# Kernel optimization log

Measured on AMD Instinct MI355X. Metric: run time of the kernel, lower is better.

The kernel has to match this reference:

```python
import jax, jax.numpy as jnp
import numpy as np

N_NODES = 40000
N_EDGES = 640000
D = 128
N_GRAPHS = 64


def gcn_conv(x, W, b, edge_index):
    """PyG-style GCNConv: add self-loops, symmetric norm, linear, scatter-add."""
    n = x.shape[0]
    loops = jnp.arange(n, dtype=edge_index.dtype)
    src = jnp.concatenate([edge_index[0], loops])  # message sources (x_j)
    dst = jnp.concatenate([edge_index[1], loops])  # aggregation targets
    # deg computed over targets (col) with unit edge weights, incl. self-loops
    deg = jax.ops.segment_sum(jnp.ones_like(src, dtype=x.dtype), dst, num_segments=n)
    dinv = jnp.where(deg > 0, jax.lax.rsqrt(jnp.maximum(deg, 1.0)), 0.0)
    norm = dinv[src] * dinv[dst]  # [E+N]
    h = x @ W  # [N, d_out]
    out = jax.ops.segment_sum(norm[:, None] * h[src], dst, num_segments=n)
    return out + b


def global_mean_pool(x, batch, num_graphs):
    summed = jax.ops.segment_sum(x, batch, num_segments=num_graphs)
    counts = jax.ops.segment_sum(jnp.ones((x.shape[0],), x.dtype), batch, num_segments=num_graphs)
    return summed / jnp.maximum(counts, 1.0)[:, None]


def setup_inputs() -> dict:
    key = jax.random.key(0)
    ks = jax.random.split(key, 6)
    x = jax.random.normal(ks[0], (N_NODES, D), dtype=jnp.float32)
    edge_index = jax.random.randint(ks[1], (2, N_EDGES), 0, N_NODES)
    batch = jnp.sort(jax.random.randint(ks[2], (N_NODES,), 0, N_GRAPHS))
    s = 1.0 / np.sqrt(D)
    W1 = jax.random.normal(ks[3], (D, D), dtype=jnp.float32) * s
    W2 = jax.random.normal(ks[4], (D, D), dtype=jnp.float32) * s
    b1 = jnp.zeros((D,), jnp.float32)
    b2 = jnp.zeros((D,), jnp.float32)
    return {"x": x, "edge_index": edge_index, "batch": batch,
            "W1": W1, "b1": b1, "W2": W2, "b2": b2}


def reference(x, edge_index, batch, W1, b1, W2, b2):
    h = jax.nn.relu(gcn_conv(x, W1, b1, edge_index))
    h = gcn_conv(h, W2, b2, edge_index)  # no ReLU on last layer
    return global_mean_pool(h, batch, N_GRAPHS)
```

## Files before the change

### kernel.cpp

```cpp
#include <hip/hip_runtime.h>

#define D 128
#define N_GRAPHS 64

typedef unsigned int uint32;
typedef __attribute__((ext_vector_type(8))) _Float16 f16x8;
typedef __attribute__((ext_vector_type(4))) float f32x4;

__device__ __forceinline__ float hl(uint32 u) {
    return (float)__builtin_bit_cast(_Float16, (unsigned short)(u & 0xFFFF));
}
__device__ __forceinline__ float hh(uint32 u) {
    return (float)__builtin_bit_cast(_Float16, (unsigned short)(u >> 16));
}
__device__ __forceinline__ uint32 h2pair(float a, float b) {
    unsigned short ua = __builtin_bit_cast(unsigned short, (_Float16)a);
    unsigned short ub = __builtin_bit_cast(unsigned short, (_Float16)b);
    return (uint32)ua | ((uint32)ub << 16);
}

__global__ __launch_bounds__(256) void prep_kernel(int* __restrict__ cnt,
                                                   const float* __restrict__ W1,
                                                   uint32* __restrict__ Wh, int n) {
    int i = blockIdx.x * 256 + threadIdx.x;
    if (i < n) {
        cnt[i] = 0;
    } else if (i < n + D * (D / 2)) {
        int j = i - n;
        int nn = j & 127, kd = j >> 7;
        float v0 = W1[(size_t)(2 * kd) * D + nn];
        float v1 = W1[(size_t)(2 * kd + 1) * D + nn];
        Wh[nn * 64 + kd] = h2pair(v0, v1);
    }
}


#define GBM 64

__global__ __launch_bounds__(256) void count_gemm_kernel(
    const float* __restrict__ A, const uint32* __restrict__ Wh,
    uint32* __restrict__ hb, int M, int gemmBlocks,
    const int* __restrict__ dst, int* __restrict__ cnt,
    int* __restrict__ rank, int E) {
    __shared__ uint32 lds[64 * 68];

    if (blockIdx.x >= gemmBlocks) {
        int e = (blockIdx.x - gemmBlocks) * 256 + threadIdx.x;
        if (e < E) rank[e] = atomicAdd(&cnt[dst[e]], 1);
        return;
    }

    uint32* As = lds;
    int tid = threadIdx.x;
    int row0 = blockIdx.x * GBM;

#pragma unroll
    for (int j = 0; j < 8; ++j) {
        int idx = tid + j * 256;
        int r = idx >> 5, c4 = idx & 31;
        float4 v = make_float4(0.f, 0.f, 0.f, 0.f);
        if (row0 + r < M) v = *(const float4*)&A[(size_t)(row0 + r) * D + c4 * 4];
        As[r * 68 + c4 * 2 + 0] = h2pair(v.x, v.y);
        As[r * 68 + c4 * 2 + 1] = h2pair(v.z, v.w);
    }
    __syncthreads();

    int wave = tid >> 6, lane = tid & 63;
    int quad = lane >> 4, l16 = lane & 15;
    int wr = (wave & 1) * 32;
    int wc = (wave >> 1) * 64;
    f32x4 acc[2][4];
#pragma unroll
    for (int mi = 0; mi < 2; ++mi)
#pragma unroll
        for (int ni = 0; ni < 4; ++ni) acc[mi][ni] = (f32x4){0.f, 0.f, 0.f, 0.f};

#pragma unroll
    for (int ks = 0; ks < 4; ++ks) {
        int kd = ks * 16 + quad * 4;
        f16x8 a0 = *(f16x8*)&As[(wr + l16) * 68 + kd];
        f16x8 a1 = *(f16x8*)&As[(wr + 16 + l16) * 68 + kd];
        f16x8 b0 = *(const f16x8*)&Wh[(wc + l16) * 64 + kd];
        f16x8 b1 = *(const f16x8*)&Wh[(wc + 16 + l16) * 64 + kd];
        f16x8 b2 = *(const f16x8*)&Wh[(wc + 32 + l16) * 64 + kd];
        f16x8 b3 = *(const f16x8*)&Wh[(wc + 48 + l16) * 64 + kd];
        acc[0][0] = __builtin_amdgcn_mfma_f32_16x16x32_f16(a0, b0, acc[0][0], 0, 0, 0);
        acc[0][1] = __builtin_amdgcn_mfma_f32_16x16x32_f16(a0, b1, acc[0][1], 0, 0, 0);
        acc[0][2] = __builtin_amdgcn_mfma_f32_16x16x32_f16(a0, b2, acc[0][2], 0, 0, 0);
        acc[0][3] = __builtin_amdgcn_mfma_f32_16x16x32_f16(a0, b3, acc[0][3], 0, 0, 0);
        acc[1][0] = __builtin_amdgcn_mfma_f32_16x16x32_f16(a1, b0, acc[1][0], 0, 0, 0);
        acc[1][1] = __builtin_amdgcn_mfma_f32_16x16x32_f16(a1, b1, acc[1][1], 0, 0, 0);
        acc[1][2] = __builtin_amdgcn_mfma_f32_16x16x32_f16(a1, b2, acc[1][2], 0, 0, 0);
        acc[1][3] = __builtin_amdgcn_mfma_f32_16x16x32_f16(a1, b3, acc[1][3], 0, 0, 0);
    }
    __syncthreads();

    unsigned short* cs = (unsigned short*)lds;
#pragma unroll
    for (int mi = 0; mi < 2; ++mi)
#pragma unroll
        for (int ni = 0; ni < 4; ++ni)
#pragma unroll
            for (int r = 0; r < 4; ++r) {
                int row = wr + mi * 16 + quad * 4 + r;
                int col2 = wc + ni * 16 + l16;
                cs[row * 128 + col2] =
                    __builtin_bit_cast(unsigned short, (_Float16)acc[mi][ni][r]);
            }
    __syncthreads();
#pragma unroll
    for (int j = 0; j < 4; ++j) {
        int idx = tid + j * 256;
        int r = idx >> 4, q = idx & 15;
        if (row0 + r < M)
            *(uint4*)&hb[(size_t)(row0 + r) * 64 + q * 4] = *(uint4*)&lds[r * 64 + q * 4];
    }
}


__global__ __launch_bounds__(1024) void scanA_kernel(const int* __restrict__ cnt,
                                                     int* __restrict__ rowptr,
                                                     int* __restrict__ tot,
                                                     float* __restrict__ dinv,
                                                     float* __restrict__ c,
                                                     const int* __restrict__ batch, int n) {
    __shared__ int swave[16];
    int t = threadIdx.x;
    int lane = t & 63, wave = t >> 6;
    int i = blockIdx.x * 1024 + t;
    {
        size_t f4base = (size_t)blockIdx.x * 1024 * 16;
        size_t f4lim = (size_t)n * 16;
        float4 z = make_float4(0.f, 0.f, 0.f, 0.f);
#pragma unroll
        for (int q = 0; q < 16; ++q) {
            size_t idx = f4base + (size_t)q * 1024 + t;
            if (idx < f4lim) ((float4*)c)[idx] = z;
        }
    }
    int orig = (i < n) ? cnt[i] : 0;
    int v = orig;
#pragma unroll
    for (int off = 1; off < 64; off <<= 1) {
        int u = __shfl_up(v, off, 64);
        if (lane >= off) v += u;
    }
    if (lane == 63) swave[wave] = v;
    __syncthreads();
    if (wave == 0) {
        int wv = (lane < 16) ? swave[lane] : 0;
#pragma unroll
        for (int off = 1; off < 16; off <<= 1) {
            int u = __shfl_up(wv, off, 64);
            if (lane >= off) wv += u;
        }
        if (lane < 16) swave[lane] = wv;
    }
    if (i < n) {
        float dv = rsqrtf((float)(orig + 1));
        dinv[i] = dv;
        c[(size_t)i * N_GRAPHS + batch[i]] = dv * dv;
    }
    __syncthreads();
    int incl = v + ((wave > 0) ? swave[wave - 1] : 0);
    if (i < n) rowptr[i] = incl - orig;
    if (t == 1023) tot[blockIdx.x] = incl;
}

__global__ __launch_bounds__(1024) void scanB_kernel(int* __restrict__ rowptr,
                                                     const int* __restrict__ tot,
                                                     int n, int nchunks) {
    __shared__ int soff;
    int b = blockIdx.x, t = threadIdx.x;
    if (t == 0) {
        int o = 0;
        for (int j = 0; j < b; ++j) o += tot[j];
        soff = o;
    }
    __syncthreads();
    int i = b * 1024 + t;
    if (i < n) rowptr[i] += soff;
    if (b == 0 && t == 0) {
        int o = 0;
        for (int j = 0; j < nchunks; ++j) o += tot[j];
        rowptr[n] = o;
    }
}

__global__ void fill_kernel(const int* __restrict__ src, const int* __restrict__ dst,
                            const int* __restrict__ rowptr, const int* __restrict__ rank,
                            int* __restrict__ col, int E) {
    int e = blockIdx.x * blockDim.x + threadIdx.x;
    if (e < E) col[rowptr[dst[e]] + rank[e]] = src[e];
}


__global__ __launch_bounds__(128) void agg_kernel(const uint32* __restrict__ hb,
                                                  const int* __restrict__ rowptr,
                                                  const int* __restrict__ col,
                                                  const float* __restrict__ dinv,
                                                  const float* __restrict__ bias,
                                                  const int* __restrict__ batch,
                                                  float* __restrict__ c,
                                                  uint32* __restrict__ h1, int n) {
    int tid = threadIdx.x;
    int lane32 = tid & 31;
    int slot = tid >> 5;
    int node = blockIdx.x * 4 + slot;
    if (node >= n) return;
    const uint2* __restrict__ h2 = (const uint2*)hb;

    float di = dinv[node];
    int bg = batch[node];
    float ws = di * di;
    uint2 su = h2[(size_t)node * 32 + lane32];
    float a0 = ws * hl(su.x), a1 = ws * hh(su.x);
    float a2 = ws * hl(su.y), a3 = ws * hh(su.y);

    int k = rowptr[node], end = rowptr[node + 1];
    for (; k + 8 <= end; k += 8) {
        uint2 v[8];
        float w[8];
#pragma unroll
        for (int j = 0; j < 8; ++j) {
            int s = col[k + j];
            w[j] = dinv[s] * di;
            v[j] = h2[(size_t)s * 32 + lane32];
            if (lane32 == j) atomicAdd(&c[(size_t)s * N_GRAPHS + bg], w[j]);
        }
#pragma unroll
        for (int j = 0; j < 8; ++j) {
            a0 = fmaf(w[j], hl(v[j].x), a0);
            a1 = fmaf(w[j], hh(v[j].x), a1);
            a2 = fmaf(w[j], hl(v[j].y), a2);
            a3 = fmaf(w[j], hh(v[j].y), a3);
        }
    }
    for (; k < end; ++k) {
        int s = col[k];
        float w = dinv[s] * di;
        uint2 v = h2[(size_t)s * 32 + lane32];
        if (lane32 == 0) atomicAdd(&c[(size_t)s * N_GRAPHS + bg], w);
        a0 = fmaf(w, hl(v.x), a0);
        a1 = fmaf(w, hh(v.x), a1);
        a2 = fmaf(w, hl(v.y), a2);
        a3 = fmaf(w, hh(v.y), a3);
    }

    float4 b4 = ((const float4*)bias)[lane32];
    a0 = fmaxf(a0 + b4.x, 0.f);
    a1 = fmaxf(a1 + b4.y, 0.f);
    a2 = fmaxf(a2 + b4.z, 0.f);
    a3 = fmaxf(a3 + b4.w, 0.f);
    uint2 o;
    o.x = h2pair(a0, a1);
    o.y = h2pair(a2, a3);
    ((uint2*)h1)[(size_t)node * 32 + lane32] = o;
}


#define GP_NB 256
#define GP_T 16

__global__ __launch_bounds__(256) void gp_kernel(const float* __restrict__ c,
                                                 const uint32* __restrict__ H1,
                                                 float* __restrict__ Ppart, int n) {
    __shared__ float sc[GP_T][N_GRAPHS];
    __shared__ uint32 sh[GP_T][64];
    int t = threadIdx.x;
    int b = blockIdx.x;
    int jpb = (n + GP_NB - 1) / GP_NB;
    int j0 = b * jpb;
    int j1 = min(j0 + jpb, n);
    int g0 = (t & 7) * 8;
    int f0 = (t >> 3) * 4;
    float acc[8][4];
#pragma unroll
    for (int a = 0; a < 8; ++a)
#pragma unroll
        for (int q = 0; q < 4; ++q) acc[a][q] = 0.f;

    for (int jt = j0; jt < j1; jt += GP_T) {
        int cnt = min(GP_T, j1 - jt);
        {
            int r = t >> 4, q = t & 15;
            float4 v = (r < cnt) ? *(const float4*)&c[(size_t)(jt + r) * N_GRAPHS + q * 4]
                                 : make_float4(0.f, 0.f, 0.f, 0.f);
            *(float4*)&sc[r][q * 4] = v;
        }
        {
            int r = t >> 4, q = t & 15;
            uint4 v = make_uint4(0, 0, 0, 0);
            if (r < cnt) v = *(const uint4*)&H1[(size_t)(jt + r) * 64 + q * 4];
            *(uint4*)&sh[r][q * 4] = v;
        }
        __syncthreads();
#pragma unroll
        for (int r = 0; r < GP_T; ++r) {
            float cw[8], hv[4];
            *(float4*)&cw[0] = *(float4*)&sc[r][g0];
            *(float4*)&cw[4] = *(float4*)&sc[r][g0 + 4];
            uint32 u0 = sh[r][f0 >> 1], u1 = sh[r][(f0 >> 1) + 1];
            hv[0] = hl(u0); hv[1] = hh(u0); hv[2] = hl(u1); hv[3] = hh(u1);
#pragma unroll
            for (int a = 0; a < 8; ++a)
#pragma unroll
                for (int q = 0; q < 4; ++q) acc[a][q] = fmaf(cw[a], hv[q], acc[a][q]);
        }
        __syncthreads();
    }
    float* P = &Ppart[(size_t)b * N_GRAPHS * D];
#pragma unroll
    for (int a = 0; a < 8; ++a)
        *(float4*)&P[(size_t)(g0 + a) * D + f0] =
            make_float4(acc[a][0], acc[a][1], acc[a][2], acc[a][3]);
}

__global__ __launch_bounds__(256) void out_kernel(const float* __restrict__ Ppart,
                                                  const float* __restrict__ W2,
                                                  const float* __restrict__ b2,
                                                  const int* __restrict__ batch, int n,
                                                  float* __restrict__ out) {
    __shared__ float gs[D];
    __shared__ float part[2][D];
    __shared__ float srinv;
    int g = blockIdx.x, t = threadIdx.x;
    int f = t & 127, half = t >> 7;
    if (t == 0) {
        int lo = 0, hi = n;
        while (lo < hi) { int mid = (lo + hi) >> 1; if (batch[mid] < g) lo = mid + 1; else hi = mid; }
        int lb = lo;
        int g1 = g + 1;
        lo = 0; hi = n;
        while (lo < hi) { int mid = (lo + hi) >> 1; if (batch[mid] < g1) lo = mid + 1; else hi = mid; }
        int cg = lo - lb;
        srinv = (cg > 0) ? 1.0f / (float)cg : 0.0f;
    }
    float s = 0.f;
    int b0 = half * (GP_NB / 2);
#pragma unroll 8
    for (int b = b0; b < b0 + GP_NB / 2; ++b)
        s += Ppart[((size_t)b * N_GRAPHS + g) * D + f];
    part[half][f] = s;
    __syncthreads();
    if (half == 0) gs[f] = part[0][f] + part[1][f];
    __syncthreads();
    float acc = 0.f;
    int k0 = half * (D / 2);
#pragma unroll 8
    for (int k = k0; k < k0 + D / 2; ++k) acc = fmaf(gs[k], W2[k * D + f], acc);
    part[half][f] = acc;
    __syncthreads();
    if (half == 0) {
        float a = part[0][f] + part[1][f];
        float r = srinv;
        out[g * D + f] = (r > 0.f) ? fmaf(a, r, b2[f]) : 0.f;
    }
}


extern "C" void kernel_launch(void* const* d_in, const int* in_sizes, int n_in,
                              void* d_out, int out_size, void* d_ws, size_t ws_size,
                              hipStream_t stream) {
    const float* x  = (const float*)d_in[0];
    const int*   ei = (const int*)d_in[1];
    const int*   batch = (const int*)d_in[2];
    const float* W1 = (const float*)d_in[3];
    const float* b1 = (const float*)d_in[4];
    const float* W2 = (const float*)d_in[5];
    const float* b2 = (const float*)d_in[6];
    float* out = (float*)d_out;

    const int n = in_sizes[2];
    const int E = in_sizes[1] / 2;
    const int* src = ei;
    const int* dst = ei + E;

    char* ws = (char*)d_ws;
    size_t off = 0;
    auto carve = [&](size_t bytes) {
        size_t o = off;
        off = (off + bytes + 255) & ~(size_t)255;
        return (void*)(ws + o);
    };
    int*    cnt    = (int*)carve((size_t)n * 4);
    int*    rowptr = (int*)carve((size_t)(n + 1) * 4);
    float*  dinv   = (float*)carve((size_t)n * 4);
    int*    col    = (int*)carve((size_t)E * 4);
    uint32* hb     = (uint32*)carve((size_t)n * D * 2);
    uint32* h1     = (uint32*)carve((size_t)n * D * 2);
    float*  c      = (float*)carve((size_t)n * N_GRAPHS * 4);
    int*    tot    = (int*)carve(64 * 4);
    int*    rank   = (int*)carve((size_t)E * 4);
    uint32* Wh     = (uint32*)carve((size_t)D * (D / 2) * 4);
    float*  Ppart  = (float*)hb;
    (void)ws_size;

    const int nchunks = (n + 1023) >> 10;

    prep_kernel<<<(n + D * (D / 2) + 255) / 256, 256, 0, stream>>>(cnt, W1, Wh, n);

    const int gemmBlocks = (n + GBM - 1) / GBM;
    const int countBlocks = (E + 255) / 256;
    count_gemm_kernel<<<gemmBlocks + countBlocks, 256, 0, stream>>>(
        x, Wh, hb, n, gemmBlocks, dst, cnt, rank, E);

    scanA_kernel<<<nchunks, 1024, 0, stream>>>(cnt, rowptr, tot, dinv, c, batch, n);
    scanB_kernel<<<nchunks, 1024, 0, stream>>>(rowptr, tot, n, nchunks);
    fill_kernel<<<(E + 255) / 256, 256, 0, stream>>>(src, dst, rowptr, rank, col, E);

    agg_kernel<<<(n + 3) / 4, 128, 0, stream>>>(hb, rowptr, col, dinv, b1, batch, c, h1, n);

    gp_kernel<<<GP_NB, 256, 0, stream>>>(c, h1, Ppart, n);
    out_kernel<<<N_GRAPHS, 256, 0, stream>>>(Ppart, W2, b2, batch, n, out);
}
```

Before: 228.9 us.

## Replace pooled-coefficient matrix with direct second-layer aggregation into per-graph pools

The old path folded the second aggregation into a dense node-by-graph coefficient matrix. That matrix was zeroed in the scan kernel, filled by scattered atomics inside the first aggregation and then contracted with h1 in gp_kernel. The new path drops that matrix and adds a kernel that, for each graph slice, re-walks the CSR neighbours of its nodes and sums the normalised messages into a shared-memory pool. The per-slice pool partials are then reduced in out_kernel. This removes the 10 MB zero/fill, the atomics and the dense contraction, but costs a second full edge gather over h1.

```diff
diff --git a/kernel.cpp b/kernel.cpp
--- a/kernel.cpp
+++ b/kernel.cpp
@@ -121,23 +121,11 @@
 __global__ __launch_bounds__(1024) void scanA_kernel(const int* __restrict__ cnt,
                                                      int* __restrict__ rowptr,
                                                      int* __restrict__ tot,
-                                                     float* __restrict__ dinv,
-                                                     float* __restrict__ c,
-                                                     const int* __restrict__ batch, int n) {
+                                                     float* __restrict__ dinv, int n) {
     __shared__ int swave[16];
     int t = threadIdx.x;
     int lane = t & 63, wave = t >> 6;
     int i = blockIdx.x * 1024 + t;
-    {
-        size_t f4base = (size_t)blockIdx.x * 1024 * 16;
-        size_t f4lim = (size_t)n * 16;
-        float4 z = make_float4(0.f, 0.f, 0.f, 0.f);
-#pragma unroll
-        for (int q = 0; q < 16; ++q) {
-            size_t idx = f4base + (size_t)q * 1024 + t;
-            if (idx < f4lim) ((float4*)c)[idx] = z;
-        }
-    }
     int orig = (i < n) ? cnt[i] : 0;
     int v = orig;
 #pragma unroll
@@ -156,11 +144,7 @@
         }
         if (lane < 16) swave[lane] = wv;
     }
-    if (i < n) {
-        float dv = rsqrtf((float)(orig + 1));
-        dinv[i] = dv;
-        c[(size_t)i * N_GRAPHS + batch[i]] = dv * dv;
-    }
+    if (i < n) dinv[i] = rsqrtf((float)(orig + 1));
     __syncthreads();
     int incl = v + ((wave > 0) ? swave[wave - 1] : 0);
     if (i < n) rowptr[i] = incl - orig;
@@ -200,8 +184,6 @@
                                                   const int* __restrict__ col,
                                                   const float* __restrict__ dinv,
                                                   const float* __restrict__ bias,
-                                                  const int* __restrict__ batch,
-                                                  float* __restrict__ c,
                                                   uint32* __restrict__ h1, int n) {
     int tid = threadIdx.x;
     int lane32 = tid & 31;
@@ -211,7 +193,6 @@
     const uint2* __restrict__ h2 = (const uint2*)hb;
 
     float di = dinv[node];
-    int bg = batch[node];
     float ws = di * di;
     uint2 su = h2[(size_t)node * 32 + lane32];
     float a0 = ws * hl(su.x), a1 = ws * hh(su.x);
@@ -226,7 +207,6 @@
             int s = col[k + j];
             w[j] = dinv[s] * di;
             v[j] = h2[(size_t)s * 32 + lane32];
-            if (lane32 == j) atomicAdd(&c[(size_t)s * N_GRAPHS + bg], w[j]);
         }
 #pragma unroll
         for (int j = 0; j < 8; ++j) {
@@ -240,7 +220,6 @@
         int s = col[k];
         float w = dinv[s] * di;
         uint2 v = h2[(size_t)s * 32 + lane32];
-        if (lane32 == 0) atomicAdd(&c[(size_t)s * N_GRAPHS + bg], w);
         a0 = fmaf(w, hl(v.x), a0);
         a1 = fmaf(w, hh(v.x), a1);
         a2 = fmaf(w, hl(v.y), a2);
@@ -258,62 +237,83 @@
     ((uint2*)h1)[(size_t)node * 32 + lane32] = o;
 }
 
-
-#define GP_NB 256
-#define GP_T 16
-
-__global__ __launch_bounds__(256) void gp_kernel(const float* __restrict__ c,
-                                                 const uint32* __restrict__ H1,
-                                                 float* __restrict__ Ppart, int n) {
-    __shared__ float sc[GP_T][N_GRAPHS];
-    __shared__ uint32 sh[GP_T][64];
+#define P2K 32
+
+__global__ __launch_bounds__(256) void agg2pool_kernel(const uint32* __restrict__ h1,
+                                                       const int* __restrict__ rowptr,
+                                                       const int* __restrict__ col,
+                                                       const float* __restrict__ dinv,
+                                                       const int* __restrict__ batch,
+                                                       float* __restrict__ Ppart, int n) {
+    __shared__ float pool[8][D];
+    __shared__ int srange[2];
     int t = threadIdx.x;
-    int b = blockIdx.x;
-    int jpb = (n + GP_NB - 1) / GP_NB;
-    int j0 = b * jpb;
-    int j1 = min(j0 + jpb, n);
-    int g0 = (t & 7) * 8;
-    int f0 = (t >> 3) * 4;
-    float acc[8][4];
-#pragma unroll
-    for (int a = 0; a < 8; ++a)
-#pragma unroll
-        for (int q = 0; q < 4; ++q) acc[a][q] = 0.f;
-
-    for (int jt = j0; jt < j1; jt += GP_T) {
-        int cnt = min(GP_T, j1 - jt);
-        {
-            int r = t >> 4, q = t & 15;
-            float4 v = (r < cnt) ? *(const float4*)&c[(size_t)(jt + r) * N_GRAPHS + q * 4]
-                                 : make_float4(0.f, 0.f, 0.f, 0.f);
-            *(float4*)&sc[r][q * 4] = v;
+    int g = blockIdx.x >> 5;
+    int kslice = blockIdx.x & 31;
+    int lane32 = t & 31, slot = t >> 5;
+
+    if (t == 0) {
+        int lo = 0, hi = n;
+        while (lo < hi) { int mid = (lo + hi) >> 1; if (batch[mid] < g) lo = mid + 1; else hi = mid; }
+        srange[0] = lo;
+        int g1 = g + 1;
+        lo = 0; hi = n;
+        while (lo < hi) { int mid = (lo + hi) >> 1; if (batch[mid] < g1) lo = mid + 1; else hi = mid; }
+        srange[1] = lo;
+    }
+    *(float4*)&pool[slot][lane32 * 4] = make_float4(0.f, 0.f, 0.f, 0.f);
+    __syncthreads();
+
+    int lb = srange[0], cntg = srange[1] - srange[0];
+    int a = lb + (int)(((long long)cntg * kslice) >> 5);
+    int b = lb + (int)(((long long)cntg * (kslice + 1)) >> 5);
+    const uint2* __restrict__ h2 = (const uint2*)h1;
+
+    for (int node = a + slot; node < b; node += 8) {
+        float di = dinv[node];
+        float ws = di * di;
+        uint2 su = h2[(size_t)node * 32 + lane32];
+        float a0 = ws * hl(su.x), a1 = ws * hh(su.x);
+        float a2 = ws * hl(su.y), a3 = ws * hh(su.y);
+
+        int k = rowptr[node], end = rowptr[node + 1];
+        for (; k + 8 <= end; k += 8) {
+            uint2 v[8];
+            float w[8];
+#pragma unroll
+            for (int j = 0; j < 8; ++j) {
+                int s = col[k + j];
+                w[j] = dinv[s] * di;
+                v[j] = h2[(size_t)s * 32 + lane32];
+            }
+#pragma unroll
+            for (int j = 0; j < 8; ++j) {
+                a0 = fmaf(w[j], hl(v[j].x), a0);
+                a1 = fmaf(w[j], hh(v[j].x), a1);
+                a2 = fmaf(w[j], hl(v[j].y), a2);
+                a3 = fmaf(w[j], hh(v[j].y), a3);
+            }
         }
-        {
-            int r = t >> 4, q = t & 15;
-            uint4 v = make_uint4(0, 0, 0, 0);
-            if (r < cnt) v = *(const uint4*)&H1[(size_t)(jt + r) * 64 + q * 4];
-            *(uint4*)&sh[r][q * 4] = v;
+        for (; k < end; ++k) {
+            int s = col[k];
+            float w = dinv[s] * di;
+            uint2 v = h2[(size_t)s * 32 + lane32];
+            a0 = fmaf(w, hl(v.x), a0);
+            a1 = fmaf(w, hh(v.x), a1);
+            a2 = fmaf(w, hl(v.y), a2);
+            a3 = fmaf(w, hh(v.y), a3);
         }
-        __syncthreads();
-#pragma unroll
-        for (int r = 0; r < GP_T; ++r) {
-            float cw[8], hv[4];
-            *(float4*)&cw[0] = *(float4*)&sc[r][g0];
-            *(float4*)&cw[4] = *(float4*)&sc[r][g0 + 4];
-            uint32 u0 = sh[r][f0 >> 1], u1 = sh[r][(f0 >> 1) + 1];
-            hv[0] = hl(u0); hv[1] = hh(u0); hv[2] = hl(u1); hv[3] = hh(u1);
-#pragma unroll
-            for (int a = 0; a < 8; ++a)
-#pragma unroll
-                for (int q = 0; q < 4; ++q) acc[a][q] = fmaf(cw[a], hv[q], acc[a][q]);
-        }
-        __syncthreads();
-    }
-    float* P = &Ppart[(size_t)b * N_GRAPHS * D];
-#pragma unroll
-    for (int a = 0; a < 8; ++a)
-        *(float4*)&P[(size_t)(g0 + a) * D + f0] =
-            make_float4(acc[a][0], acc[a][1], acc[a][2], acc[a][3]);
+        float4 p = *(float4*)&pool[slot][lane32 * 4];
+        p.x += a0; p.y += a1; p.z += a2; p.w += a3;
+        *(float4*)&pool[slot][lane32 * 4] = p;
+    }
+    __syncthreads();
+    if (t < D) {
+        float s = 0.f;
+#pragma unroll
+        for (int sl = 0; sl < 8; ++sl) s += pool[sl][t];
+        Ppart[(size_t)blockIdx.x * D + t] = s;
+    }
 }
 
 __global__ __launch_bounds__(256) void out_kernel(const float* __restrict__ Ppart,
@@ -337,10 +337,10 @@
         srinv = (cg > 0) ? 1.0f / (float)cg : 0.0f;
     }
     float s = 0.f;
-    int b0 = half * (GP_NB / 2);
-#pragma unroll 8
-    for (int b = b0; b < b0 + GP_NB / 2; ++b)
-        s += Ppart[((size_t)b * N_GRAPHS + g) * D + f];
+    int j0 = half * (P2K / 2);
+#pragma unroll
+    for (int j = j0; j < j0 + P2K / 2; ++j)
+        s += Ppart[((size_t)g * P2K + j) * D + f];
     part[half][f] = s;
     __syncthreads();
     if (half == 0) gs[f] = part[0][f] + part[1][f];
@@ -389,7 +389,6 @@
     int*    col    = (int*)carve((size_t)E * 4);
     uint32* hb     = (uint32*)carve((size_t)n * D * 2);
     uint32* h1     = (uint32*)carve((size_t)n * D * 2);
-    float*  c      = (float*)carve((size_t)n * N_GRAPHS * 4);
     int*    tot    = (int*)carve(64 * 4);
     int*    rank   = (int*)carve((size_t)E * 4);
     uint32* Wh     = (uint32*)carve((size_t)D * (D / 2) * 4);
@@ -405,12 +404,13 @@
     count_gemm_kernel<<<gemmBlocks + countBlocks, 256, 0, stream>>>(
         x, Wh, hb, n, gemmBlocks, dst, cnt, rank, E);
 
-    scanA_kernel<<<nchunks, 1024, 0, stream>>>(cnt, rowptr, tot, dinv, c, batch, n);
+    scanA_kernel<<<nchunks, 1024, 0, stream>>>(cnt, rowptr, tot, dinv, n);
     scanB_kernel<<<nchunks, 1024, 0, stream>>>(rowptr, tot, n, nchunks);
     fill_kernel<<<(E + 255) / 256, 256, 0, stream>>>(src, dst, rowptr, rank, col, E);
 
-    agg_kernel<<<(n + 3) / 4, 128, 0, stream>>>(hb, rowptr, col, dinv, b1, batch, c, h1, n);
-
-    gp_kernel<<<GP_NB, 256, 0, stream>>>(c, h1, Ppart, n);
+    agg_kernel<<<(n + 3) / 4, 128, 0, stream>>>(hb, rowptr, col, dinv, b1, h1, n);
+
+    agg2pool_kernel<<<N_GRAPHS * P2K, 256, 0, stream>>>(h1, rowptr, col, dinv, batch,
+                                                        Ppart, n);
     out_kernel<<<N_GRAPHS, 256, 0, stream>>>(Ppart, W2, b2, batch, n, out);
 }
```

Result: faster. 201.2 us (-12.1%).
